# Optimization experiments

Measured on AMD Instinct MI355X. Metric: run time of the kernel, lower is better.

Reference implementation:

```python
import jax, jax.numpy as jnp
import numpy as np

B, H, L, T, V = 32, 1024, 128, 127, 32000


def setup_inputs() -> dict:
    key = jax.random.key(0)
    ks = jax.random.split(key, 16)
    s = 1.0 / np.sqrt(H)
    return {
        "word_indices": jax.random.randint(ks[0], (B,), 0, V),
        "last_hidden": jax.random.normal(ks[1], (1, B, H), jnp.float32),
        "tanh_hidden": jax.random.normal(ks[2], (B, H), jnp.float32),
        "tree_output": jax.random.normal(ks[3], (T, B, H), jnp.float32),
        "seq_output": jax.random.normal(ks[4], (L, B, H), jnp.float32),
        "numNode": jax.random.randint(ks[5], (B,), 0, T),
        "emb_table": jax.random.normal(ks[6], (V, H), jnp.float32) * 0.02,
        "W_ih": jax.random.uniform(ks[7], (4 * H, H), jnp.float32, -s, s),
        "W_hh": jax.random.uniform(ks[8], (4 * H, H), jnp.float32, -s, s),
        "b_ih": jax.random.uniform(ks[9], (4 * H,), jnp.float32, -s, s),
        "b_hh": jax.random.uniform(ks[10], (4 * H,), jnp.float32, -s, s),
        "W_comb": jax.random.uniform(ks[11], (H, 2 * H), jnp.float32, -s, s),
        "b_comb": jax.random.uniform(ks[12], (H,), jnp.float32, -s, s),
        "W_out": jax.random.uniform(ks[13], (V, H), jnp.float32, -s, s),
        "b_out": jax.random.uniform(ks[14], (V,), jnp.float32, -s, s),
    }


def _lstm_cell(x, h, c, W_ih, W_hh, b_ih, b_hh):
    gates = x @ W_ih.T + b_ih + h @ W_hh.T + b_hh  # (B, 4H)
    i, f, g, o = jnp.split(gates, 4, axis=-1)      # torch gate order i,f,g,o
    i, f, o = jax.nn.sigmoid(i), jax.nn.sigmoid(f), jax.nn.sigmoid(o)
    c1 = f * c + i * jnp.tanh(g)
    return o * jnp.tanh(c1), c1


def reference(word_indices, last_hidden, tanh_hidden, tree_output, seq_output,
              numNode, emb_table, W_ih, W_hh, b_ih, b_hh, W_comb, b_comb,
              W_out, b_out):
    tree = jnp.transpose(tree_output, (1, 0, 2))  # (B,T,H)
    seq = jnp.transpose(seq_output, (1, 0, 2))    # (B,L,H)
    lhidden = last_hidden[0]                       # (B,H)

    # LSTM step (skipped if all word indices are 0 == begin token)
    emb = emb_table[word_indices]                  # (B,H)
    h0 = lhidden + tanh_hidden
    c0 = jnp.zeros_like(h0)
    h1, _ = _lstm_cell(emb, h0, c0, W_ih, W_hh, b_ih, b_hh)
    is_begin = jnp.sum(word_indices) == 0
    cur = jnp.where(is_begin, lhidden, h1)         # (B,H)

    # Ragged attention over concat(seq[:numLeaf], tree[:numNode]) via masking
    enc = jnp.concatenate([seq, tree], axis=1)     # (B, L+T, H)
    pos = jnp.arange(L + T)
    numLeaf = numNode + 1
    mask = jnp.where(pos[None, :] < L,
                     pos[None, :] < numLeaf[:, None],
                     (pos[None, :] - L) < numNode[:, None])  # (B, L+T)
    scores = jnp.einsum('bh,bth->bt', cur, enc)
    scores = jnp.where(mask, scores, -1e30)
    w = jax.nn.softmax(scores, axis=1)
    context = jnp.einsum('bt,bth->bh', w, enc)     # (B,H)

    tanh_h = jnp.tanh(jnp.concatenate([cur, context], axis=1) @ W_comb.T + b_comb)
    out_vec = tanh_h @ W_out.T + b_out             # (B,V)
    prob = jax.nn.softmax(out_vec, axis=0)         # NOTE: dim=0 as in source
    return prob, cur, tanh_h, context
```

## Files before the change

kernel.cpp:

```cpp
#include <hip/hip_runtime.h>

#define BB 32
#define HH 1024
#define LL 128
#define TT 127
#define VV 32000
#define NT 255

typedef __attribute__((ext_vector_type(8))) short bf16x8;
typedef __attribute__((ext_vector_type(4))) float f32x4;

static __device__ __forceinline__ short f2bf(float f) {
  unsigned u = __builtin_bit_cast(unsigned, f);
  u += 0x7fffu + ((u >> 16) & 1u);
  return (short)(u >> 16);
}

static __device__ __forceinline__ bf16x8 load_cvt8(const float* __restrict__ p) {
  f32x4 a = *(const f32x4*)p;
  f32x4 b = *(const f32x4*)(p + 4);
  bf16x8 r;
  r[0]=f2bf(a[0]); r[1]=f2bf(a[1]); r[2]=f2bf(a[2]); r[3]=f2bf(a[3]);
  r[4]=f2bf(b[0]); r[5]=f2bf(b[1]); r[6]=f2bf(b[2]); r[7]=f2bf(b[3]);
  return r;
}

static __device__ __forceinline__ bf16x8 load_add_cvt8(const float* __restrict__ p,
                                                       const float* __restrict__ q) {
  f32x4 a = *(const f32x4*)p, a2 = *(const f32x4*)(p + 4);
  f32x4 b = *(const f32x4*)q, b2 = *(const f32x4*)(q + 4);
  bf16x8 r;
  r[0]=f2bf(a[0]+b[0]); r[1]=f2bf(a[1]+b[1]); r[2]=f2bf(a[2]+b[2]); r[3]=f2bf(a[3]+b[3]);
  r[4]=f2bf(a2[0]+b2[0]); r[5]=f2bf(a2[1]+b2[1]); r[6]=f2bf(a2[2]+b2[2]); r[7]=f2bf(a2[3]+b2[3]);
  return r;
}

__global__ __launch_bounds__(64) void k_gates(
    const int* __restrict__ wi, const float* __restrict__ lh,
    const float* __restrict__ th, const float* __restrict__ emb,
    const float* __restrict__ W_ih, const float* __restrict__ W_hh,
    float* __restrict__ pgates)
{
  int lane = threadIdx.x;
  int tile = blockIdx.x >> 2;
  int ks   = blockIdx.x & 3;
  int al = lane & 15, ah = lane >> 4;
  int cg = tile * 16 + al;
  int g  = (cg < 1024) ? cg : cg + 1024;
  const float* W = (ks < 2) ? W_ih : W_hh;
  int kbase = (ks & 1) * 512;
  const float* Arow = W + (size_t)g * HH + kbase + ah * 8;
  int b_lo = al, b_hi = al + 16;
  f32x4 acc_lo = {0.f,0.f,0.f,0.f}, acc_hi = {0.f,0.f,0.f,0.f};

  if (ks < 2) {
    const float* e_lo = emb + (size_t)wi[b_lo] * HH + kbase + ah * 8;
    const float* e_hi = emb + (size_t)wi[b_hi] * HH + kbase + ah * 8;
    #pragma unroll 4
    for (int kk = 0; kk < 16; ++kk) {
      bf16x8 a  = load_cvt8(Arow + kk * 32);
      bf16x8 bl = load_cvt8(e_lo + kk * 32);
      bf16x8 bh = load_cvt8(e_hi + kk * 32);
      acc_lo = __builtin_amdgcn_mfma_f32_16x16x32_bf16(a, bl, acc_lo, 0, 0, 0);
      acc_hi = __builtin_amdgcn_mfma_f32_16x16x32_bf16(a, bh, acc_hi, 0, 0, 0);
    }
  } else {
    const float* p_lo = lh + b_lo * HH + kbase + ah * 8;
    const float* q_lo = th + b_lo * HH + kbase + ah * 8;
    const float* p_hi = lh + b_hi * HH + kbase + ah * 8;
    const float* q_hi = th + b_hi * HH + kbase + ah * 8;
    #pragma unroll 4
    for (int kk = 0; kk < 16; ++kk) {
      bf16x8 a  = load_cvt8(Arow + kk * 32);
      bf16x8 bl = load_add_cvt8(p_lo + kk * 32, q_lo + kk * 32);
      bf16x8 bh = load_add_cvt8(p_hi + kk * 32, q_hi + kk * 32);
      acc_lo = __builtin_amdgcn_mfma_f32_16x16x32_bf16(a, bl, acc_lo, 0, 0, 0);
      acc_hi = __builtin_amdgcn_mfma_f32_16x16x32_bf16(a, bh, acc_hi, 0, 0, 0);
    }
  }
  float* outp = pgates + ((size_t)ks * 3072 + tile * 16) * 32;
  #pragma unroll
  for (int j = 0; j < 4; ++j) {
    int row = ah * 4 + j;
    outp[row * 32 + al]      = acc_lo[j];
    outp[row * 32 + al + 16] = acc_hi[j];
  }
}

__global__ __launch_bounds__(256) void k_cell(
    const float* __restrict__ pgates, const float* __restrict__ b_ih,
    const float* __restrict__ b_hh, const int* __restrict__ wi,
    const float* __restrict__ lh, float* __restrict__ cur_ws,
    float* __restrict__ out_cur)
{
  __shared__ int s_begin;
  if (threadIdx.x == 0) {
    int s = 0;
    #pragma unroll
    for (int i = 0; i < BB; ++i) s += wi[i];
    s_begin = (s == 0);
  }
  __syncthreads();
  int b = threadIdx.x & 31;
  int h = blockIdx.x * 8 + (threadIdx.x >> 5);
  float iv = 0.f, gv = 0.f, ov = 0.f;
  #pragma unroll
  for (int ks = 0; ks < 4; ++ks) {
    const float* p = pgates + (size_t)ks * 3072 * 32;
    iv += p[(size_t)h * 32 + b];
    gv += p[(size_t)(1024 + h) * 32 + b];
    ov += p[(size_t)(2048 + h) * 32 + b];
  }
  iv += b_ih[h] + b_hh[h];
  gv += b_ih[2048 + h] + b_hh[2048 + h];
  ov += b_ih[3072 + h] + b_hh[3072 + h];
  float ig = 1.f / (1.f + __expf(-iv));
  float og = 1.f / (1.f + __expf(-ov));
  float c1 = ig * tanhf(gv);
  float h1 = og * tanhf(c1);
  float c  = s_begin ? lh[b * HH + h] : h1;
  cur_ws[b * HH + h] = c;
  out_cur[b * HH + h] = c;
}

__global__ __launch_bounds__(256) void k_scores(
    const float* __restrict__ cur, const float* __restrict__ seq,
    const float* __restrict__ tree, const int* __restrict__ numNode,
    float* __restrict__ scores)
{
  int lane = threadIdx.x & 63;
  int gw = blockIdx.x * 4 + (threadIdx.x >> 6);
  if (gw >= BB * NT) return;
  int b = gw & 31, t = gw >> 5;
  int nn = numNode[b];
  int tl    = (t < LL) ? t : (t - LL);
  int limit = (t < LL) ? (nn + 1) : nn;
  if (tl >= limit) { if (lane == 0) scores[b * NT + t] = -1e30f; return; }
  const float* row = (t < LL) ? (seq + ((size_t)t * BB + b) * HH)
                              : (tree + ((size_t)(t - LL) * BB + b) * HH);
  const float* c = cur + b * HH;
  float acc = 0.f;
  #pragma unroll
  for (int ch = 0; ch < 4; ++ch) {
    int k = ch * 256 + lane * 4;
    f32x4 e = *(const f32x4*)(row + k);
    f32x4 q = *(const f32x4*)(c + k);
    acc += e[0]*q[0] + e[1]*q[1] + e[2]*q[2] + e[3]*q[3];
  }
  #pragma unroll
  for (int off = 32; off; off >>= 1) acc += __shfl_xor(acc, off);
  if (lane == 0) scores[b * NT + t] = acc;
}

__global__ __launch_bounds__(256) void k_context(
    const float* __restrict__ scores, const float* __restrict__ seq,
    const float* __restrict__ tree, const int* __restrict__ numNode,
    float* __restrict__ ctx_ws, float* __restrict__ out_ctx)
{
  int b  = blockIdx.x >> 2;
  int hc = blockIdx.x & 3;
  int tid = threadIdx.x;
  __shared__ float w[256];
  __shared__ float red[4];
  float s = (tid < NT) ? scores[b * NT + tid] : -1e30f;
  float m = s;
  #pragma unroll
  for (int off = 32; off; off >>= 1) m = fmaxf(m, __shfl_xor(m, off));
  if ((tid & 63) == 0) red[tid >> 6] = m;
  __syncthreads();
  m = fmaxf(fmaxf(red[0], red[1]), fmaxf(red[2], red[3]));
  float e = (tid < NT) ? __expf(s - m) : 0.f;
  float z = e;
  #pragma unroll
  for (int off = 32; off; off >>= 1) z += __shfl_xor(z, off);
  __syncthreads();
  if ((tid & 63) == 0) red[tid >> 6] = z;
  __syncthreads();
  z = red[0] + red[1] + red[2] + red[3];
  w[tid] = e / z;
  __syncthreads();

  int h = hc * 256 + tid;
  int nn = numNode[b];
  int nl = nn + 1;
  float acc = 0.f;
  #pragma unroll 4
  for (int t = 0; t < nl; ++t) acc += w[t] * seq[((size_t)t * BB + b) * HH + h];
  #pragma unroll 4
  for (int t = 0; t < nn; ++t) acc += w[LL + t] * tree[((size_t)t * BB + b) * HH + h];
  ctx_ws[b * HH + h] = acc;
  out_ctx[b * HH + h] = acc;
}

__global__ __launch_bounds__(64) void k_comb(
    const float* __restrict__ W_comb, const float* __restrict__ cur,
    const float* __restrict__ ctx, float* __restrict__ pcomb)
{
  int lane = threadIdx.x;
  int tile = blockIdx.x >> 2;
  int ks   = blockIdx.x & 3;
  int al = lane & 15, ah = lane >> 4;
  int m = tile * 16 + al;
  int kbase = ks * 512;
  const float* Arow = W_comb + (size_t)m * 2048 + kbase + ah * 8;
  const float* X = (ks < 2) ? cur : ctx;
  int xkb = kbase & 1023;
  const float* xlo = X + al * HH + xkb + ah * 8;
  const float* xhi = X + (al + 16) * HH + xkb + ah * 8;
  f32x4 acc_lo = {0.f,0.f,0.f,0.f}, acc_hi = {0.f,0.f,0.f,0.f};
  #pragma unroll 4
  for (int kk = 0; kk < 16; ++kk) {
    bf16x8 a  = load_cvt8(Arow + kk * 32);
    bf16x8 bl = load_cvt8(xlo + kk * 32);
    bf16x8 bh = load_cvt8(xhi + kk * 32);
    acc_lo = __builtin_amdgcn_mfma_f32_16x16x32_bf16(a, bl, acc_lo, 0, 0, 0);
    acc_hi = __builtin_amdgcn_mfma_f32_16x16x32_bf16(a, bh, acc_hi, 0, 0, 0);
  }
  float* outp = pcomb + ((size_t)ks * 1024 + tile * 16) * 32;
  #pragma unroll
  for (int j = 0; j < 4; ++j) {
    int row = ah * 4 + j;
    outp[row * 32 + al]      = acc_lo[j];
    outp[row * 32 + al + 16] = acc_hi[j];
  }
}

__global__ __launch_bounds__(256) void k_combred(
    const float* __restrict__ pcomb, const float* __restrict__ b_comb,
    float* __restrict__ out_th, unsigned short* __restrict__ thb)
{
  int b = threadIdx.x & 31;
  int m = blockIdx.x * 8 + (threadIdx.x >> 5);
  float v = 0.f;
  #pragma unroll
  for (int ks = 0; ks < 4; ++ks) v += pcomb[((size_t)ks * 1024 + m) * 32 + b];
  v = tanhf(v + b_comb[m]);
  out_th[b * HH + m] = v;
  thb[b * HH + m] = (unsigned short)f2bf(v);
}

__global__ __launch_bounds__(64) void k_wout(
    const float* __restrict__ W_out, const unsigned short* __restrict__ thb,
    float* __restrict__ vt)
{
  int lane = threadIdx.x;
  int tile = blockIdx.x;
  int al = lane & 15, ah = lane >> 4;
  size_t row = (size_t)tile * 16 + al;
  const float* Arow = W_out + row * HH + ah * 8;
  const unsigned short* blo = thb + al * HH + ah * 8;
  const unsigned short* bhi = thb + (al + 16) * HH + ah * 8;
  f32x4 acc_lo = {0.f,0.f,0.f,0.f}, acc_hi = {0.f,0.f,0.f,0.f};
  #pragma unroll 4
  for (int kk = 0; kk < 32; ++kk) {
    bf16x8 a  = load_cvt8(Arow + kk * 32);
    bf16x8 bl = *(const bf16x8*)(blo + kk * 32);
    bf16x8 bh = *(const bf16x8*)(bhi + kk * 32);
    acc_lo = __builtin_amdgcn_mfma_f32_16x16x32_bf16(a, bl, acc_lo, 0, 0, 0);
    acc_hi = __builtin_amdgcn_mfma_f32_16x16x32_bf16(a, bh, acc_hi, 0, 0, 0);
  }
  float* outp = vt + (size_t)tile * 16 * 32;
  #pragma unroll
  for (int j = 0; j < 4; ++j) {
    int r = ah * 4 + j;
    outp[r * 32 + al]      = acc_lo[j];
    outp[r * 32 + al + 16] = acc_hi[j];
  }
}

__global__ __launch_bounds__(256) void k_psoftmax(
    const float* __restrict__ vt, float* __restrict__ prob)
{
  int v = blockIdx.x * 256 + threadIdx.x;
  const float* r = vt + (size_t)v * 32;
  float x[32];
  #pragma unroll
  for (int i = 0; i < 8; ++i) {
    f32x4 t = *(const f32x4*)(r + i * 4);
    x[i*4+0] = t[0]; x[i*4+1] = t[1]; x[i*4+2] = t[2]; x[i*4+3] = t[3];
  }
  float m = x[0];
  #pragma unroll
  for (int i = 1; i < 32; ++i) m = fmaxf(m, x[i]);
  float z = 0.f;
  #pragma unroll
  for (int i = 0; i < 32; ++i) { x[i] = __expf(x[i] - m); z += x[i]; }
  float inv = 1.f / z;
  #pragma unroll
  for (int i = 0; i < 32; ++i) prob[(size_t)i * VV + v] = x[i] * inv;
}

extern "C" void kernel_launch(void* const* d_in, const int* in_sizes, int n_in,
                              void* d_out, int out_size, void* d_ws, size_t ws_size,
                              hipStream_t stream) {
  const int*   wi    = (const int*)d_in[0];
  const float* lh    = (const float*)d_in[1];
  const float* thid  = (const float*)d_in[2];
  const float* tree  = (const float*)d_in[3];
  const float* seq   = (const float*)d_in[4];
  const int*   nn    = (const int*)d_in[5];
  const float* emb   = (const float*)d_in[6];
  const float* Wih   = (const float*)d_in[7];
  const float* Whh   = (const float*)d_in[8];
  const float* bih   = (const float*)d_in[9];
  const float* bhh   = (const float*)d_in[10];
  const float* Wcomb = (const float*)d_in[11];
  const float* bcomb = (const float*)d_in[12];
  const float* Wout  = (const float*)d_in[13];

  float* out = (float*)d_out;
  float* ws  = (float*)d_ws;
  float* pgates = ws;
  float* pcomb  = ws + 393216;
  float* cur    = ws + 524288;
  float* ctx    = ws + 557056;
  float* scores = ws + 589824;
  unsigned short* thb = (unsigned short*)(ws + 598016);
  float* vt     = ws + 614400;

  float* o_prob = out;
  float* o_cur  = out + 1024000;
  float* o_th   = out + 1056768;
  float* o_ctx  = out + 1089536;

  k_gates   <<<dim3(768),  dim3(64),  0, stream>>>(wi, lh, thid, emb, Wih, Whh, pgates);
  k_cell    <<<dim3(128),  dim3(256), 0, stream>>>(pgates, bih, bhh, wi, lh, cur, o_cur);
  k_scores  <<<dim3(2040), dim3(256), 0, stream>>>(cur, seq, tree, nn, scores);
  k_context <<<dim3(128),  dim3(256), 0, stream>>>(scores, seq, tree, nn, ctx, o_ctx);
  k_comb    <<<dim3(256),  dim3(64),  0, stream>>>(Wcomb, cur, ctx, pcomb);
  k_combred <<<dim3(128),  dim3(256), 0, stream>>>(pcomb, bcomb, o_th, thb);
  k_wout    <<<dim3(2000), dim3(64),  0, stream>>>(Wout, thb, vt);
  k_psoftmax<<<dim3(125),  dim3(256), 0, stream>>>(vt, o_prob);
}
```

Before: 373.5 us.

## Fuse all stages into one cooperative persistent kernel with grid syncs

Replaces the eight separate kernel launches with a single cooperative kernel of 256 blocks that runs each stage in turn, separated by grid.sync barriers. Split-K is made finer in several stages: gates and comb use 8 K-slices instead of 4, context is split over 4 time chunks and reduced later, and W_out is split into two K-halves. The aim is to remove launch overhead and the gaps between kernels. In exchange it adds grid-wide barrier cost, leaves only 256 blocks resident, and increases partial-sum traffic.

```diff
diff --git a/kernel.cpp b/kernel.cpp
--- a/kernel.cpp
+++ b/kernel.cpp
@@ -1,4 +1,7 @@
 #include <hip/hip_runtime.h>
+#include <hip/hip_cooperative_groups.h>
+
+namespace cg = cooperative_groups;
 
 #define BB 32
 #define HH 1024
@@ -9,6 +12,8 @@
 
 typedef __attribute__((ext_vector_type(8))) short bf16x8;
 typedef __attribute__((ext_vector_type(4))) float f32x4;
+
+#define MFMA(a, b, c) __builtin_amdgcn_mfma_f32_16x16x32_bf16((a), (b), (c), 0, 0, 0)
 
 static __device__ __forceinline__ short f2bf(float f) {
   unsigned u = __builtin_bit_cast(unsigned, f);
@@ -35,259 +40,268 @@
   return r;
 }
 
-__global__ __launch_bounds__(64) void k_gates(
+static __device__ __forceinline__ bf16x8 sum4_cvt8(const float* __restrict__ pctx,
+                                                   int b, int col) {
+  const float* p = pctx + (size_t)b * HH + col;
+  f32x4 a0 = *(const f32x4*)p,           a1 = *(const f32x4*)(p + 4);
+  f32x4 b0 = *(const f32x4*)(p + 32768), b1 = *(const f32x4*)(p + 32772);
+  f32x4 c0 = *(const f32x4*)(p + 65536), c1 = *(const f32x4*)(p + 65540);
+  f32x4 d0 = *(const f32x4*)(p + 98304), d1 = *(const f32x4*)(p + 98308);
+  bf16x8 r;
+  r[0]=f2bf(a0[0]+b0[0]+c0[0]+d0[0]); r[1]=f2bf(a0[1]+b0[1]+c0[1]+d0[1]);
+  r[2]=f2bf(a0[2]+b0[2]+c0[2]+d0[2]); r[3]=f2bf(a0[3]+b0[3]+c0[3]+d0[3]);
+  r[4]=f2bf(a1[0]+b1[0]+c1[0]+d1[0]); r[5]=f2bf(a1[1]+b1[1]+c1[1]+d1[1]);
+  r[6]=f2bf(a1[2]+b1[2]+c1[2]+d1[2]); r[7]=f2bf(a1[3]+b1[3]+c1[3]+d1[3]);
+  return r;
+}
+
+__global__ __launch_bounds__(256) void k_mega(
     const int* __restrict__ wi, const float* __restrict__ lh,
-    const float* __restrict__ th, const float* __restrict__ emb,
-    const float* __restrict__ W_ih, const float* __restrict__ W_hh,
-    float* __restrict__ pgates)
+    const float* __restrict__ th, const float* __restrict__ tree,
+    const float* __restrict__ seq, const int* __restrict__ nnp,
+    const float* __restrict__ emb, const float* __restrict__ Wih,
+    const float* __restrict__ Whh, const float* __restrict__ bih,
+    const float* __restrict__ bhh, const float* __restrict__ Wcomb,
+    const float* __restrict__ bcomb, const float* __restrict__ Wout,
+    float* __restrict__ out, float* __restrict__ ws)
 {
-  int lane = threadIdx.x;
-  int tile = blockIdx.x >> 2;
-  int ks   = blockIdx.x & 3;
-  int al = lane & 15, ah = lane >> 4;
-  int cg = tile * 16 + al;
-  int g  = (cg < 1024) ? cg : cg + 1024;
-  const float* W = (ks < 2) ? W_ih : W_hh;
-  int kbase = (ks & 1) * 512;
-  const float* Arow = W + (size_t)g * HH + kbase + ah * 8;
-  int b_lo = al, b_hi = al + 16;
-  f32x4 acc_lo = {0.f,0.f,0.f,0.f}, acc_hi = {0.f,0.f,0.f,0.f};
-
-  if (ks < 2) {
-    const float* e_lo = emb + (size_t)wi[b_lo] * HH + kbase + ah * 8;
-    const float* e_hi = emb + (size_t)wi[b_hi] * HH + kbase + ah * 8;
+  cg::grid_group grid = cg::this_grid();
+  const int lane = threadIdx.x & 63;
+  const int widx = threadIdx.x >> 6;
+  const int gw   = blockIdx.x * 4 + widx;
+  const int al   = lane & 15, ah = lane >> 4;
+
+  float* pgates = ws;
+  float* pcomb  = ws + 786432;
+  float* pctx   = ws + 1048576;
+  float* cur    = ws + 1179648;
+  float* scores = ws + 1212416;
+  unsigned short* thb = (unsigned short*)(ws + 1220608);
+  float* vt2    = ws + 1236992;
+
+  float* o_prob = out;
+  float* o_cur  = out + 1024000;
+  float* o_th   = out + 1056768;
+  float* o_ctx  = out + 1089536;
+
+  __shared__ float sw[4][64];
+
+  for (int task = gw; task < 1536; task += 1024) {
+    int tile = task >> 3, ks = task & 7;
+    int cgi = tile * 16 + al;
+    int g = (cgi < 1024) ? cgi : cgi + 1024;
+    const float* W = (ks < 4) ? Wih : Whh;
+    int kbase = (ks & 3) * 256;
+    const float* Arow = W + (size_t)g * HH + kbase + ah * 8;
+    f32x4 acc_lo = {0.f,0.f,0.f,0.f}, acc_hi = {0.f,0.f,0.f,0.f};
+    if (ks < 4) {
+      const float* e_lo = emb + (size_t)wi[al] * HH + kbase + ah * 8;
+      const float* e_hi = emb + (size_t)wi[al + 16] * HH + kbase + ah * 8;
+      #pragma unroll
+      for (int kk = 0; kk < 8; ++kk) {
+        bf16x8 a = load_cvt8(Arow + kk * 32);
+        acc_lo = MFMA(a, load_cvt8(e_lo + kk * 32), acc_lo);
+        acc_hi = MFMA(a, load_cvt8(e_hi + kk * 32), acc_hi);
+      }
+    } else {
+      const float* p_lo = lh + al * HH + kbase + ah * 8;
+      const float* q_lo = th + al * HH + kbase + ah * 8;
+      const float* p_hi = lh + (al + 16) * HH + kbase + ah * 8;
+      const float* q_hi = th + (al + 16) * HH + kbase + ah * 8;
+      #pragma unroll
+      for (int kk = 0; kk < 8; ++kk) {
+        bf16x8 a = load_cvt8(Arow + kk * 32);
+        acc_lo = MFMA(a, load_add_cvt8(p_lo + kk * 32, q_lo + kk * 32), acc_lo);
+        acc_hi = MFMA(a, load_add_cvt8(p_hi + kk * 32, q_hi + kk * 32), acc_hi);
+      }
+    }
+    float* op = pgates + ((size_t)ks * 3072 + tile * 16) * 32;
+    #pragma unroll
+    for (int j = 0; j < 4; ++j) {
+      int r = ah * 4 + j;
+      op[r * 32 + al]      = acc_lo[j];
+      op[r * 32 + al + 16] = acc_hi[j];
+    }
+  }
+  grid.sync();
+
+  if (gw < 512) {
+    int idx = gw * 64 + lane;
+    int b = idx & 31, h = idx >> 5;
+    float iv = 0.f, gv = 0.f, ov = 0.f;
+    #pragma unroll
+    for (int ks = 0; ks < 8; ++ks) {
+      const float* p = pgates + (size_t)ks * 3072 * 32;
+      iv += p[(size_t)h * 32 + b];
+      gv += p[(size_t)(1024 + h) * 32 + b];
+      ov += p[(size_t)(2048 + h) * 32 + b];
+    }
+    iv += bih[h] + bhh[h];
+    gv += bih[2048 + h] + bhh[2048 + h];
+    ov += bih[3072 + h] + bhh[3072 + h];
+    float ig = 1.f / (1.f + __expf(-iv));
+    float og = 1.f / (1.f + __expf(-ov));
+    float c1 = ig * tanhf(gv);
+    float h1 = og * tanhf(c1);
+    int s = 0;
+    #pragma unroll
+    for (int i = 0; i < BB; ++i) s += wi[i];
+    float c = (s == 0) ? lh[b * HH + h] : h1;
+    cur[b * HH + h] = c;
+    o_cur[b * HH + h] = c;
+  }
+  grid.sync();
+
+  for (int task = gw; task < BB * NT; task += 1024) {
+    int b = task & 31, t = task >> 5;
+    int nn = nnp[b];
+    int tl    = (t < LL) ? t : (t - LL);
+    int limit = (t < LL) ? (nn + 1) : nn;
+    if (tl >= limit) { if (lane == 0) scores[b * NT + t] = -1e30f; continue; }
+    const float* row = (t < LL) ? (seq + ((size_t)t * BB + b) * HH)
+                                : (tree + ((size_t)(t - LL) * BB + b) * HH);
+    const float* c = cur + b * HH;
+    float acc = 0.f;
+    #pragma unroll
+    for (int ch = 0; ch < 4; ++ch) {
+      int k = ch * 256 + lane * 4;
+      f32x4 e = *(const f32x4*)(row + k);
+      f32x4 q = *(const f32x4*)(c + k);
+      acc += e[0]*q[0] + e[1]*q[1] + e[2]*q[2] + e[3]*q[3];
+    }
+    #pragma unroll
+    for (int off = 32; off; off >>= 1) acc += __shfl_xor(acc, off);
+    if (lane == 0) scores[b * NT + t] = acc;
+  }
+  grid.sync();
+
+  for (int task = gw; task < 2048; task += 1024) {
+    int b = task >> 6, rem = task & 63, hc = rem >> 2, tc = rem & 3;
+    const float* sb = scores + b * NT;
+    float s0 = sb[lane];
+    float s1 = sb[64 + lane];
+    float s2 = sb[128 + lane];
+    float s3 = (lane < 63) ? sb[192 + lane] : -1e30f;
+    float m = fmaxf(fmaxf(s0, s1), fmaxf(s2, s3));
+    #pragma unroll
+    for (int off = 32; off; off >>= 1) m = fmaxf(m, __shfl_xor(m, off));
+    float z = __expf(s0 - m) + __expf(s1 - m) + __expf(s2 - m)
+            + ((lane < 63) ? __expf(s3 - m) : 0.f);
+    #pragma unroll
+    for (int off = 32; off; off >>= 1) z += __shfl_xor(z, off);
+    int t = tc * 64 + lane;
+    float sown = (t < NT) ? sb[t] : -1e30f;
+    sw[widx][lane] = __expf(sown - m) / z;
+    __syncthreads();
+    int h = hc * 64 + lane;
+    int ntt = (tc == 3) ? 63 : 64;
+    const float* base = (tc < 2)
+        ? seq + ((size_t)(tc * 64) * BB + b) * HH + h
+        : tree + ((size_t)(tc * 64 - LL) * BB + b) * HH + h;
+    float acc = 0.f;
+    #pragma unroll 8
+    for (int tt = 0; tt < ntt; ++tt)
+      acc += sw[widx][tt] * base[(size_t)tt * (BB * HH)];
+    pctx[((size_t)tc * BB + b) * HH + h] = acc;
+    __syncthreads();
+  }
+  grid.sync();
+
+  if (gw < 512) {
+    int tile = gw >> 3, ks = gw & 7;
+    int mm = tile * 16 + al;
+    int kbase = (ks & 3) * 256;
+    const float* Arow = Wcomb + (size_t)mm * 2048 + ks * 256 + ah * 8;
+    f32x4 acc_lo = {0.f,0.f,0.f,0.f}, acc_hi = {0.f,0.f,0.f,0.f};
+    if (ks < 4) {
+      const float* xlo = cur + al * HH + kbase + ah * 8;
+      const float* xhi = cur + (al + 16) * HH + kbase + ah * 8;
+      #pragma unroll
+      for (int kk = 0; kk < 8; ++kk) {
+        bf16x8 a = load_cvt8(Arow + kk * 32);
+        acc_lo = MFMA(a, load_cvt8(xlo + kk * 32), acc_lo);
+        acc_hi = MFMA(a, load_cvt8(xhi + kk * 32), acc_hi);
+      }
+    } else {
+      int xc = kbase + ah * 8;
+      #pragma unroll
+      for (int kk = 0; kk < 8; ++kk) {
+        bf16x8 a = load_cvt8(Arow + kk * 32);
+        acc_lo = MFMA(a, sum4_cvt8(pctx, al,      xc + kk * 32), acc_lo);
+        acc_hi = MFMA(a, sum4_cvt8(pctx, al + 16, xc + kk * 32), acc_hi);
+      }
+    }
+    float* op = pcomb + ((size_t)ks * 1024 + tile * 16) * 32;
+    #pragma unroll
+    for (int j = 0; j < 4; ++j) {
+      int r = ah * 4 + j;
+      op[r * 32 + al]      = acc_lo[j];
+      op[r * 32 + al + 16] = acc_hi[j];
+    }
+  }
+  grid.sync();
+
+  if (gw < 512) {
+    int idx = gw * 64 + lane;
+    int b = idx & 31, mm = idx >> 5;
+    float v = 0.f;
+    #pragma unroll
+    for (int ks = 0; ks < 8; ++ks) v += pcomb[((size_t)ks * 1024 + mm) * 32 + b];
+    v = tanhf(v + bcomb[mm]);
+    o_th[b * HH + mm] = v;
+    thb[b * HH + mm] = (unsigned short)f2bf(v);
+    size_t ci = (size_t)b * HH + mm;
+    o_ctx[ci] = pctx[ci] + pctx[32768 + ci] + pctx[65536 + ci] + pctx[98304 + ci];
+  }
+  grid.sync();
+
+  for (int task = gw; task < 4000; task += 1024) {
+    int tile = task >> 1, half = task & 1;
+    size_t row = (size_t)tile * 16 + al;
+    const float* Arow = Wout + row * HH + half * 512 + ah * 8;
+    const unsigned short* blo = thb + al * HH + half * 512 + ah * 8;
+    const unsigned short* bhi = thb + (al + 16) * HH + half * 512 + ah * 8;
+    f32x4 acc_lo = {0.f,0.f,0.f,0.f}, acc_hi = {0.f,0.f,0.f,0.f};
     #pragma unroll 4
     for (int kk = 0; kk < 16; ++kk) {
       bf16x8 a  = load_cvt8(Arow + kk * 32);
-      bf16x8 bl = load_cvt8(e_lo + kk * 32);
-      bf16x8 bh = load_cvt8(e_hi + kk * 32);
-      acc_lo = __builtin_amdgcn_mfma_f32_16x16x32_bf16(a, bl, acc_lo, 0, 0, 0);
-      acc_hi = __builtin_amdgcn_mfma_f32_16x16x32_bf16(a, bh, acc_hi, 0, 0, 0);
-    }
-  } else {
-    const float* p_lo = lh + b_lo * HH + kbase + ah * 8;
-    const float* q_lo = th + b_lo * HH + kbase + ah * 8;
-    const float* p_hi = lh + b_hi * HH + kbase + ah * 8;
-    const float* q_hi = th + b_hi * HH + kbase + ah * 8;
-    #pragma unroll 4
-    for (int kk = 0; kk < 16; ++kk) {
-      bf16x8 a  = load_cvt8(Arow + kk * 32);
-      bf16x8 bl = load_add_cvt8(p_lo + kk * 32, q_lo + kk * 32);
-      bf16x8 bh = load_add_cvt8(p_hi + kk * 32, q_hi + kk * 32);
-      acc_lo = __builtin_amdgcn_mfma_f32_16x16x32_bf16(a, bl, acc_lo, 0, 0, 0);
-      acc_hi = __builtin_amdgcn_mfma_f32_16x16x32_bf16(a, bh, acc_hi, 0, 0, 0);
-    }
-  }
-  float* outp = pgates + ((size_t)ks * 3072 + tile * 16) * 32;
-  #pragma unroll
-  for (int j = 0; j < 4; ++j) {
-    int row = ah * 4 + j;
-    outp[row * 32 + al]      = acc_lo[j];
-    outp[row * 32 + al + 16] = acc_hi[j];
-  }
-}
-
-__global__ __launch_bounds__(256) void k_cell(
-    const float* __restrict__ pgates, const float* __restrict__ b_ih,
-    const float* __restrict__ b_hh, const int* __restrict__ wi,
-    const float* __restrict__ lh, float* __restrict__ cur_ws,
-    float* __restrict__ out_cur)
-{
-  __shared__ int s_begin;
-  if (threadIdx.x == 0) {
-    int s = 0;
-    #pragma unroll
-    for (int i = 0; i < BB; ++i) s += wi[i];
-    s_begin = (s == 0);
-  }
-  __syncthreads();
-  int b = threadIdx.x & 31;
-  int h = blockIdx.x * 8 + (threadIdx.x >> 5);
-  float iv = 0.f, gv = 0.f, ov = 0.f;
-  #pragma unroll
-  for (int ks = 0; ks < 4; ++ks) {
-    const float* p = pgates + (size_t)ks * 3072 * 32;
-    iv += p[(size_t)h * 32 + b];
-    gv += p[(size_t)(1024 + h) * 32 + b];
-    ov += p[(size_t)(2048 + h) * 32 + b];
-  }
-  iv += b_ih[h] + b_hh[h];
-  gv += b_ih[2048 + h] + b_hh[2048 + h];
-  ov += b_ih[3072 + h] + b_hh[3072 + h];
-  float ig = 1.f / (1.f + __expf(-iv));
-  float og = 1.f / (1.f + __expf(-ov));
-  float c1 = ig * tanhf(gv);
-  float h1 = og * tanhf(c1);
-  float c  = s_begin ? lh[b * HH + h] : h1;
-  cur_ws[b * HH + h] = c;
-  out_cur[b * HH + h] = c;
-}
-
-__global__ __launch_bounds__(256) void k_scores(
-    const float* __restrict__ cur, const float* __restrict__ seq,
-    const float* __restrict__ tree, const int* __restrict__ numNode,
-    float* __restrict__ scores)
-{
-  int lane = threadIdx.x & 63;
-  int gw = blockIdx.x * 4 + (threadIdx.x >> 6);
-  if (gw >= BB * NT) return;
-  int b = gw & 31, t = gw >> 5;
-  int nn = numNode[b];
-  int tl    = (t < LL) ? t : (t - LL);
-  int limit = (t < LL) ? (nn + 1) : nn;
-  if (tl >= limit) { if (lane == 0) scores[b * NT + t] = -1e30f; return; }
-  const float* row = (t < LL) ? (seq + ((size_t)t * BB + b) * HH)
-                              : (tree + ((size_t)(t - LL) * BB + b) * HH);
-  const float* c = cur + b * HH;
-  float acc = 0.f;
-  #pragma unroll
-  for (int ch = 0; ch < 4; ++ch) {
-    int k = ch * 256 + lane * 4;
-    f32x4 e = *(const f32x4*)(row + k);
-    f32x4 q = *(const f32x4*)(c + k);
-    acc += e[0]*q[0] + e[1]*q[1] + e[2]*q[2] + e[3]*q[3];
-  }
-  #pragma unroll
-  for (int off = 32; off; off >>= 1) acc += __shfl_xor(acc, off);
-  if (lane == 0) scores[b * NT + t] = acc;
-}
-
-__global__ __launch_bounds__(256) void k_context(
-    const float* __restrict__ scores, const float* __restrict__ seq,
-    const float* __restrict__ tree, const int* __restrict__ numNode,
-    float* __restrict__ ctx_ws, float* __restrict__ out_ctx)
-{
-  int b  = blockIdx.x >> 2;
-  int hc = blockIdx.x & 3;
-  int tid = threadIdx.x;
-  __shared__ float w[256];
-  __shared__ float red[4];
-  float s = (tid < NT) ? scores[b * NT + tid] : -1e30f;
-  float m = s;
-  #pragma unroll
-  for (int off = 32; off; off >>= 1) m = fmaxf(m, __shfl_xor(m, off));
-  if ((tid & 63) == 0) red[tid >> 6] = m;
-  __syncthreads();
-  m = fmaxf(fmaxf(red[0], red[1]), fmaxf(red[2], red[3]));
-  float e = (tid < NT) ? __expf(s - m) : 0.f;
-  float z = e;
-  #pragma unroll
-  for (int off = 32; off; off >>= 1) z += __shfl_xor(z, off);
-  __syncthreads();
-  if ((tid & 63) == 0) red[tid >> 6] = z;
-  __syncthreads();
-  z = red[0] + red[1] + red[2] + red[3];
-  w[tid] = e / z;
-  __syncthreads();
-
-  int h = hc * 256 + tid;
-  int nn = numNode[b];
-  int nl = nn + 1;
-  float acc = 0.f;
-  #pragma unroll 4
-  for (int t = 0; t < nl; ++t) acc += w[t] * seq[((size_t)t * BB + b) * HH + h];
-  #pragma unroll 4
-  for (int t = 0; t < nn; ++t) acc += w[LL + t] * tree[((size_t)t * BB + b) * HH + h];
-  ctx_ws[b * HH + h] = acc;
-  out_ctx[b * HH + h] = acc;
-}
-
-__global__ __launch_bounds__(64) void k_comb(
-    const float* __restrict__ W_comb, const float* __restrict__ cur,
-    const float* __restrict__ ctx, float* __restrict__ pcomb)
-{
-  int lane = threadIdx.x;
-  int tile = blockIdx.x >> 2;
-  int ks   = blockIdx.x & 3;
-  int al = lane & 15, ah = lane >> 4;
-  int m = tile * 16 + al;
-  int kbase = ks * 512;
-  const float* Arow = W_comb + (size_t)m * 2048 + kbase + ah * 8;
-  const float* X = (ks < 2) ? cur : ctx;
-  int xkb = kbase & 1023;
-  const float* xlo = X + al * HH + xkb + ah * 8;
-  const float* xhi = X + (al + 16) * HH + xkb + ah * 8;
-  f32x4 acc_lo = {0.f,0.f,0.f,0.f}, acc_hi = {0.f,0.f,0.f,0.f};
-  #pragma unroll 4
-  for (int kk = 0; kk < 16; ++kk) {
-    bf16x8 a  = load_cvt8(Arow + kk * 32);
-    bf16x8 bl = load_cvt8(xlo + kk * 32);
-    bf16x8 bh = load_cvt8(xhi + kk * 32);
-    acc_lo = __builtin_amdgcn_mfma_f32_16x16x32_bf16(a, bl, acc_lo, 0, 0, 0);
-    acc_hi = __builtin_amdgcn_mfma_f32_16x16x32_bf16(a, bh, acc_hi, 0, 0, 0);
-  }
-  float* outp = pcomb + ((size_t)ks * 1024 + tile * 16) * 32;
-  #pragma unroll
-  for (int j = 0; j < 4; ++j) {
-    int row = ah * 4 + j;
-    outp[row * 32 + al]      = acc_lo[j];
-    outp[row * 32 + al + 16] = acc_hi[j];
-  }
-}
-
-__global__ __launch_bounds__(256) void k_combred(
-    const float* __restrict__ pcomb, const float* __restrict__ b_comb,
-    float* __restrict__ out_th, unsigned short* __restrict__ thb)
-{
-  int b = threadIdx.x & 31;
-  int m = blockIdx.x * 8 + (threadIdx.x >> 5);
-  float v = 0.f;
-  #pragma unroll
-  for (int ks = 0; ks < 4; ++ks) v += pcomb[((size_t)ks * 1024 + m) * 32 + b];
-  v = tanhf(v + b_comb[m]);
-  out_th[b * HH + m] = v;
-  thb[b * HH + m] = (unsigned short)f2bf(v);
-}
-
-__global__ __launch_bounds__(64) void k_wout(
-    const float* __restrict__ W_out, const unsigned short* __restrict__ thb,
-    float* __restrict__ vt)
-{
-  int lane = threadIdx.x;
-  int tile = blockIdx.x;
-  int al = lane & 15, ah = lane >> 4;
-  size_t row = (size_t)tile * 16 + al;
-  const float* Arow = W_out + row * HH + ah * 8;
-  const unsigned short* blo = thb + al * HH + ah * 8;
-  const unsigned short* bhi = thb + (al + 16) * HH + ah * 8;
-  f32x4 acc_lo = {0.f,0.f,0.f,0.f}, acc_hi = {0.f,0.f,0.f,0.f};
-  #pragma unroll 4
-  for (int kk = 0; kk < 32; ++kk) {
-    bf16x8 a  = load_cvt8(Arow + kk * 32);
-    bf16x8 bl = *(const bf16x8*)(blo + kk * 32);
-    bf16x8 bh = *(const bf16x8*)(bhi + kk * 32);
-    acc_lo = __builtin_amdgcn_mfma_f32_16x16x32_bf16(a, bl, acc_lo, 0, 0, 0);
-    acc_hi = __builtin_amdgcn_mfma_f32_16x16x32_bf16(a, bh, acc_hi, 0, 0, 0);
-  }
-  float* outp = vt + (size_t)tile * 16 * 32;
-  #pragma unroll
-  for (int j = 0; j < 4; ++j) {
-    int r = ah * 4 + j;
-    outp[r * 32 + al]      = acc_lo[j];
-    outp[r * 32 + al + 16] = acc_hi[j];
-  }
-}
-
-__global__ __launch_bounds__(256) void k_psoftmax(
-    const float* __restrict__ vt, float* __restrict__ prob)
-{
-  int v = blockIdx.x * 256 + threadIdx.x;
-  const float* r = vt + (size_t)v * 32;
-  float x[32];
-  #pragma unroll
-  for (int i = 0; i < 8; ++i) {
-    f32x4 t = *(const f32x4*)(r + i * 4);
-    x[i*4+0] = t[0]; x[i*4+1] = t[1]; x[i*4+2] = t[2]; x[i*4+3] = t[3];
-  }
-  float m = x[0];
-  #pragma unroll
-  for (int i = 1; i < 32; ++i) m = fmaxf(m, x[i]);
-  float z = 0.f;
-  #pragma unroll
-  for (int i = 0; i < 32; ++i) { x[i] = __expf(x[i] - m); z += x[i]; }
-  float inv = 1.f / z;
-  #pragma unroll
-  for (int i = 0; i < 32; ++i) prob[(size_t)i * VV + v] = x[i] * inv;
+      bf16x8 bl = *(const bf16x8*)(blo + kk * 32);
+      bf16x8 bh = *(const bf16x8*)(bhi + kk * 32);
+      acc_lo = MFMA(a, bl, acc_lo);
+      acc_hi = MFMA(a, bh, acc_hi);
+    }
+    float* op = vt2 + (size_t)half * 1024000 + (size_t)tile * 16 * 32;
+    #pragma unroll
+    for (int j = 0; j < 4; ++j) {
+      int r = ah * 4 + j;
+      op[r * 32 + al]      = acc_lo[j];
+      op[r * 32 + al + 16] = acc_hi[j];
+    }
+  }
+  grid.sync();
+
+  if (gw < 500) {
+    int v = gw * 64 + lane;
+    const float* r0 = vt2 + (size_t)v * 32;
+    const float* r1 = vt2 + 1024000 + (size_t)v * 32;
+    float x[32];
+    #pragma unroll
+    for (int i = 0; i < 8; ++i) {
+      f32x4 t0 = *(const f32x4*)(r0 + i * 4);
+      f32x4 t1 = *(const f32x4*)(r1 + i * 4);
+      x[i*4+0] = t0[0]+t1[0]; x[i*4+1] = t0[1]+t1[1];
+      x[i*4+2] = t0[2]+t1[2]; x[i*4+3] = t0[3]+t1[3];
+    }
+    float m = x[0];
+    #pragma unroll
+    for (int i = 1; i < 32; ++i) m = fmaxf(m, x[i]);
+    float z = 0.f;
+    #pragma unroll
+    for (int i = 0; i < 32; ++i) { x[i] = __expf(x[i] - m); z += x[i]; }
+    float inv = 1.f / z;
+    #pragma unroll
+    for (int i = 0; i < 32; ++i) o_prob[(size_t)i * VV + v] = x[i] * inv;
+  }
 }
 
 extern "C" void kernel_launch(void* const* d_in, const int* in_sizes, int n_in,
@@ -298,7 +312,7 @@
   const float* thid  = (const float*)d_in[2];
   const float* tree  = (const float*)d_in[3];
   const float* seq   = (const float*)d_in[4];
-  const int*   nn    = (const int*)d_in[5];
+  const int*   nnp   = (const int*)d_in[5];
   const float* emb   = (const float*)d_in[6];
   const float* Wih   = (const float*)d_in[7];
   const float* Whh   = (const float*)d_in[8];
@@ -308,27 +322,14 @@
   const float* bcomb = (const float*)d_in[12];
   const float* Wout  = (const float*)d_in[13];
 
-  float* out = (float*)d_out;
-  float* ws  = (float*)d_ws;
-  float* pgates = ws;
-  float* pcomb  = ws + 393216;
-  float* cur    = ws + 524288;
-  float* ctx    = ws + 557056;
-  float* scores = ws + 589824;
-  unsigned short* thb = (unsigned short*)(ws + 598016);
-  float* vt     = ws + 614400;
-
-  float* o_prob = out;
-  float* o_cur  = out + 1024000;
-  float* o_th   = out + 1056768;
-  float* o_ctx  = out + 1089536;
-
-  k_gates   <<<dim3(768),  dim3(64),  0, stream>>>(wi, lh, thid, emb, Wih, Whh, pgates);
-  k_cell    <<<dim3(128),  dim3(256), 0, stream>>>(pgates, bih, bhh, wi, lh, cur, o_cur);
-  k_scores  <<<dim3(2040), dim3(256), 0, stream>>>(cur, seq, tree, nn, scores);
-  k_context <<<dim3(128),  dim3(256), 0, stream>>>(scores, seq, tree, nn, ctx, o_ctx);
-  k_comb    <<<dim3(256),  dim3(64),  0, stream>>>(Wcomb, cur, ctx, pcomb);
-  k_combred <<<dim3(128),  dim3(256), 0, stream>>>(pcomb, bcomb, o_th, thb);
-  k_wout    <<<dim3(2000), dim3(64),  0, stream>>>(Wout, thb, vt);
-  k_psoftmax<<<dim3(125),  dim3(256), 0, stream>>>(vt, o_prob);
-}
+  float* outp = (float*)d_out;
+  float* wsp  = (float*)d_ws;
+
+  void* args[] = {
+    (void*)&wi, (void*)&lh, (void*)&thid, (void*)&tree, (void*)&seq,
+    (void*)&nnp, (void*)&emb, (void*)&Wih, (void*)&Whh, (void*)&bih,
+    (void*)&bhh, (void*)&Wcomb, (void*)&bcomb, (void*)&Wout,
+    (void*)&outp, (void*)&wsp
+  };
+  hipLaunchCooperativeKernel((void*)k_mega, dim3(256), dim3(256), args, 0, stream);
+}
```

Measured after the change: 624.9 us. 1.67x slower.
